# Optimization experiments

Measured on AMD Instinct MI355X. Metric: run time of the kernel, lower is better.

## Reference

```python
import jax, jax.numpy as jnp
import numpy as np

EPS = 1e-12

def _l2norm(x):
    n = jnp.sqrt(jnp.sum(x * x, axis=-1, keepdims=True))
    return x / jnp.maximum(n, EPS)

def setup_inputs() -> dict:
    key = jax.random.key(0)
    k1, k2 = jax.random.split(key)
    B, S, H = 32, 256, 768
    return {
        "query_embs": jax.random.normal(k1, (B, S, H), dtype=jnp.float32),
        "key_embs": jax.random.normal(k2, (B, S, H), dtype=jnp.float32),
        "q_mask": jnp.ones((B, S), dtype=jnp.float32),
        "k_mask": jnp.ones((B, S), dtype=jnp.float32),
        "alpha_raw": jnp.asarray(1.0, dtype=jnp.float32),
        "logit_scale": jnp.asarray(0.0, dtype=jnp.float32),  # log(1.0)
    }

def reference(query_embs, key_embs, q_mask, k_mask, alpha_raw, logit_scale):
    # query_embs, key_embs: (B, S, H); masks: (B, S)
    S = query_embs.shape[1]
    q = _l2norm(query_embs)
    k = _l2norm(key_embs)
    # all-pairs token similarity: (B, B, S, T)
    sim = jnp.einsum('ish,jth->ijst', q, k)
    # distance-decay weighting (do_distance=True, exp_decay=True)
    alpha = jax.nn.softplus(alpha_raw)
    pos = jnp.arange(S, dtype=jnp.float32)
    dist = jnp.abs(pos[:, None] - pos[None, :])  # (S, S)
    sim = sim * jnp.exp(-alpha * dist)
    # validity mask: (B, B, S, T)
    valid = (q_mask[:, None, :, None] * k_mask[None, :, None, :]) > 0
    scale = jnp.exp(logit_scale)
    neg_inf = jnp.float32(-jnp.inf)
    logits = jnp.where(valid, scale * sim, neg_inf)
    all_inf = jnp.all(logits == neg_inf, axis=-1, keepdims=True)
    safe_logits = jnp.where(all_inf, 0.0, logits)
    p = jax.nn.softmax(safe_logits, axis=-1)
    p = jnp.where(all_inf, 0.0, p)
    # softmax-weighted key aggregation: (B, B, S, H)
    agg = jnp.einsum('ijst,jth->ijsh', p, k)
    # per-token cosine score, masked mean over query tokens
    scores = jnp.einsum('ish,ijsh->ijs', q, agg) * q_mask[:, None, :]
    denom = jnp.clip(jnp.sum(q_mask, axis=-1, keepdims=True), 1.0, None)
    return jnp.sum(scores, axis=-1) / denom  # (B, B)
```

## Files before the change

### kernel.cpp

```cpp
#include <hip/hip_runtime.h>
#include <cmath>

#define BB 32
#define SS 256
#define HH 768

typedef __attribute__((ext_vector_type(8))) short bfrag8;
typedef __attribute__((ext_vector_type(4))) float accf4;

__device__ __forceinline__ unsigned short f2bf(float x) {
    unsigned int b = __float_as_uint(x);
    return (unsigned short)((b + 0x7FFFu + ((b >> 16) & 1u)) >> 16);
}

__device__ __forceinline__ float bf2f(unsigned short u) {
    return __uint_as_float(((unsigned int)u) << 16);
}

__device__ __forceinline__ void gload16(const void* g, void* l) {
    __builtin_amdgcn_global_load_lds((const __attribute__((address_space(1))) void*)g,
                                     (__attribute__((address_space(3))) void*)l, 16, 0, 0);
}


__global__ __launch_bounds__(256)
void normcvt_kernel(const float* __restrict__ Q, const float* __restrict__ K,
                    unsigned short* __restrict__ qws, unsigned short* __restrict__ kws) {
    const int wave = threadIdx.x >> 6, lane = threadIdx.x & 63;
    const bool isQ = blockIdx.x < 2048;
    const int rr = (blockIdx.x * 4 + wave) & 8191;
    const float4* src4 = isQ ? (const float4*)(Q + (size_t)rr * HH)
                             : (const float4*)(K + (size_t)rr * HH);
    float4 vv[3]; float s = 0.f;
#pragma unroll
    for (int c = 0; c < 3; ++c) {
        vv[c] = src4[lane + 64 * c];
        s += vv[c].x * vv[c].x + vv[c].y * vv[c].y + vv[c].z * vv[c].z + vv[c].w * vv[c].w;
    }
#pragma unroll
    for (int off = 1; off < 64; off <<= 1) s += __shfl_xor(s, off);
    float inv = 1.f / fmaxf(sqrtf(s), 1e-12f);

    const int b = rr >> 8, srow = rr & 255;
    unsigned short* dst = isQ ? qws : kws;
    const int e = (lane & 7) * 4;
    const int fp8 = (((e >> 3) ^ ((srow >> 1) & 3)) << 3) + (e & 7);
#pragma unroll
    for (int c = 0; c < 3; ++c) {
        int kc = (lane >> 3) + 8 * c;
        ushort4 o;
        o.x = f2bf(vv[c].x * inv); o.y = f2bf(vv[c].y * inv);
        o.z = f2bf(vv[c].z * inv); o.w = f2bf(vv[c].w * inv);
        *(ushort4*)(dst + (((size_t)b * 24 + kc) * 256 + srow) * 32 + fp8) = o;
    }
}

__global__ __launch_bounds__(256)
void ksum_kernel(const unsigned short* __restrict__ kws, const float* __restrict__ kmask,
                 unsigned short* __restrict__ ksumB) {
    __shared__ float red[4][8][4];
    const int j = blockIdx.x / 24, kc = blockIdx.x - j * 24;
    const int lane = threadIdx.x & 63, wv = threadIdx.x >> 6;
    const int tg = threadIdx.x >> 3;
    const int ec = threadIdx.x & 7;
    const unsigned short* base = kws + ((size_t)(j * 24 + kc)) * 8192;
    const float* km = kmask + j * SS;
    const int f = ec >> 1, off4 = (ec & 1) * 4;
    float s0 = 0.f, s1 = 0.f, s2 = 0.f, s3 = 0.f;
    for (int t = tg; t < 256; t += 32) {
        if (km[t] > 0.f) {
            int pos = ((f ^ ((t >> 1) & 3)) << 3) + off4;
            ushort4 v = *(const ushort4*)(base + t * 32 + pos);
            s0 += bf2f(v.x); s1 += bf2f(v.y); s2 += bf2f(v.z); s3 += bf2f(v.w);
        }
    }
#pragma unroll
    for (int off = 8; off < 64; off <<= 1) {
        s0 += __shfl_xor(s0, off); s1 += __shfl_xor(s1, off);
        s2 += __shfl_xor(s2, off); s3 += __shfl_xor(s3, off);
    }
    if ((lane >> 3) == 0) {
        red[wv][ec][0] = s0; red[wv][ec][1] = s1; red[wv][ec][2] = s2; red[wv][ec][3] = s3;
    }
    __syncthreads();
    if (threadIdx.x < 32) {
        int e2 = threadIdx.x;
        float tot = red[0][e2 >> 2][e2 & 3] + red[1][e2 >> 2][e2 & 3]
                  + red[2][e2 >> 2][e2 & 3] + red[3][e2 >> 2][e2 & 3];
        ksumB[(size_t)(j * 24 + kc) * 32 + e2] = f2bf(tot);
    }
}

__global__ __launch_bounds__(512, 2)
void mfma_kernel(const unsigned short* __restrict__ qws, const unsigned short* __restrict__ kws,
                 const float* __restrict__ qmask, const float* __restrict__ kmask,
                 const float* __restrict__ araw_p, const float* __restrict__ lscale_p,
                 const unsigned short* __restrict__ ksumB, float* __restrict__ out) {
    __shared__ __align__(16) short lq[2][8192];
    __shared__ __align__(16) short lk[2][8192];
    __shared__ __align__(16) short lKsum[2][768];
    __shared__ float sKm[2][256];
    __shared__ float wtab[13];
    __shared__ float sRed[8][2];
    __shared__ float sPart[8][2];
    __shared__ float sKcnt[2], sQden[2];

    const int tid = threadIdx.x;
    const int lane = tid & 63, w = tid >> 6;
    const int quad = lane >> 4, col = lane & 15;
    const int li = w >> 2, wq = w & 3;

    const int xcd = (int)blockIdx.x & 7, bidx = (int)blockIdx.x >> 3;
    const int ip = (xcd >> 1) * 4 + (bidx >> 3);
    const int jp = (xcd & 1) * 8 + (bidx & 7);
    const int i0 = ip * 2, j0 = jp * 2;

    const float alpha = log1pf(__expf(araw_p[0]));
    const float scale = __expf(lscale_p[0]);

    const int half = tid >> 8, hidx = tid & 255;
    float aq = qmask[(i0 + half) * SS + hidx];
    float km = kmask[(j0 + half) * SS + hidx];
    sKm[half][hidx] = km;
    float c = (km > 0.f) ? 1.f : 0.f;
#pragma unroll
    for (int off = 1; off < 64; off <<= 1) { aq += __shfl_xor(aq, off); c += __shfl_xor(c, off); }
    if (lane == 0) { sRed[w][0] = aq; sRed[w][1] = c; }
    if (tid < 13) wtab[tid] = __expf(-alpha * (float)tid);
    if (tid < 384) {
        const int jj = (tid >= 192) ? 1 : 0, e = tid - jj * 192;
        ((ushort4*)&lKsum[jj][0])[e] = ((const ushort4*)(ksumB + (size_t)(j0 + jj) * HH))[e];
    }
    __syncthreads();
    if (tid == 0) {
        sQden[0] = fmaxf(sRed[0][0] + sRed[1][0] + sRed[2][0] + sRed[3][0], 1.f);
        sQden[1] = fmaxf(sRed[4][0] + sRed[5][0] + sRed[6][0] + sRed[7][0], 1.f);
        sKcnt[0] = sRed[0][1] + sRed[1][1] + sRed[2][1] + sRed[3][1];
        sKcnt[1] = sRed[4][1] + sRed[5][1] + sRed[6][1] + sRed[7][1];
    }

    accf4 acc[2][4][3];
    accf4 accB[2][4];
#pragma unroll
    for (int lj = 0; lj < 2; ++lj) {
#pragma unroll
        for (int a = 0; a < 4; ++a) {
            accB[lj][a] = (accf4)0.f;
#pragma unroll
            for (int b = 0; b < 3; ++b) acc[lj][a][b] = (accf4)0.f;
        }
    }

    const unsigned short* psrc = (w < 4)
        ? qws + (size_t)(i0 + ((w >> 1) & 1)) * 24 * 8192
        : kws + (size_t)(j0 + ((w >> 1) & 1)) * 24 * 8192;
    unsigned short* pdst = (unsigned short*)((w < 4) ? lq[(w >> 1) & 1] : lk[(w >> 1) & 1])
                           + (w & 1) * 4096;
    const unsigned short* ssrc = psrc + (w & 1) * 4096 + lane * 8;

    const int perm8 = ((quad ^ ((col >> 1) & 3)) << 3);

    for (int kc = 0; kc < 24; ++kc) {
        __syncthreads();
        {
            const unsigned short* s = ssrc + (size_t)kc * 8192;
#pragma unroll
            for (int n = 0; n < 8; ++n)
                gload16(s + n * 512, pdst + n * 512);
        }
        __syncthreads();

        bfrag8 af[4];
#pragma unroll
        for (int sbl = 0; sbl < 4; ++sbl)
            af[sbl] = *(const bfrag8*)(&lq[li][(size_t)((wq * 4 + sbl) * 16 + col) * 32 + perm8]);
#pragma unroll
        for (int lj = 0; lj < 2; ++lj) {
            const bfrag8 kfrag = *(const bfrag8*)(&lKsum[lj][kc * 32 + quad * 8]);
            bfrag8 bfr[6];
#pragma unroll
            for (int u = 0; u < 6; ++u) {
                int tb = 4 * wq - 1 + u;
                if (tb >= 0 && tb <= 15)
                    bfr[u] = *(const bfrag8*)(&lk[lj][(size_t)(tb * 16 + col) * 32 + perm8]);
            }
#pragma unroll
            for (int sbl = 0; sbl < 4; ++sbl) {
                accB[lj][sbl] = __builtin_amdgcn_mfma_f32_16x16x32_bf16(
                    af[sbl], kfrag, accB[lj][sbl], 0, 0, 0);
#pragma unroll
                for (int dtb = 0; dtb < 3; ++dtb) {
                    int tb = 4 * wq + sbl - 1 + dtb;
                    if (tb >= 0 && tb <= 15)
                        acc[lj][sbl][dtb] = __builtin_amdgcn_mfma_f32_16x16x32_bf16(
                            af[sbl], bfr[sbl + dtb], acc[lj][sbl][dtb], 0, 0, 0);
                }
            }
        }
    }

    __syncthreads();
    float part[2] = {0.f, 0.f};
#pragma unroll
    for (int lj = 0; lj < 2; ++lj) {
        const float kcnt = sKcnt[lj];
#pragma unroll
        for (int sbl = 0; sbl < 4; ++sbl) {
            const int sbase = (wq * 4 + sbl) * 16 + quad * 4;
            float ns[4] = {0.f, 0.f, 0.f, 0.f}, ds[4] = {0.f, 0.f, 0.f, 0.f};
#pragma unroll
            for (int dtb = 0; dtb < 3; ++dtb) {
                int tb = wq * 4 + sbl - 1 + dtb;
                if (tb < 0 || tb > 15) continue;
                int t = tb * 16 + col;
                float kmv = sKm[lj][t];
#pragma unroll
                for (int reg = 0; reg < 4; ++reg) {
                    int st = sbase + reg;
                    int d = t - st;
                    bool ok = (d >= -11) && (d <= 12) && (kmv > 0.f);
                    int idx = d < 0 ? -d : d;
                    idx = ok ? idx : 0;
                    float raw = acc[lj][sbl][dtb][reg];
                    float e = ok ? expm1f(scale * raw * wtab[idx]) : 0.f;
                    ns[reg] = fmaf(e, raw, ns[reg]);
                    ds[reg] += e;
                }
            }
#pragma unroll
            for (int off = 1; off < 16; off <<= 1) {
#pragma unroll
                for (int reg = 0; reg < 4; ++reg) {
                    ns[reg] += __shfl_xor(ns[reg], off);
                    ds[reg] += __shfl_xor(ds[reg], off);
                }
            }
            if (col == 0) {
#pragma unroll
                for (int reg = 0; reg < 4; ++reg) {
                    int st = sbase + reg;
                    float qm = qmask[(i0 + li) * SS + st];
                    float bse = accB[lj][sbl][reg];
                    float dtot = ds[reg] + kcnt;
                    float v = (qm > 0.f && kcnt > 0.f) ? qm * (ns[reg] + bse) / dtot : 0.f;
                    part[lj] += v;
                }
            }
        }
    }
#pragma unroll
    for (int lj = 0; lj < 2; ++lj) {
        part[lj] += __shfl_xor(part[lj], 16);
        part[lj] += __shfl_xor(part[lj], 32);
    }
    if (lane == 0) { sPart[w][0] = part[0]; sPart[w][1] = part[1]; }
    __syncthreads();
    if (tid < 4) {
        const int tli = tid >> 1, tlj = tid & 1;
        float s = sPart[tli * 4 + 0][tlj] + sPart[tli * 4 + 1][tlj]
                + sPart[tli * 4 + 2][tlj] + sPart[tli * 4 + 3][tlj];
        out[(i0 + tli) * BB + (j0 + tlj)] = s / sQden[tli];
    }
}


extern "C" void kernel_launch(void* const* d_in, const int* in_sizes, int n_in,
                              void* d_out, int out_size, void* d_ws, size_t ws_size,
                              hipStream_t stream) {
    const float* Q      = (const float*)d_in[0];
    const float* K      = (const float*)d_in[1];
    const float* qmask  = (const float*)d_in[2];
    const float* kmask  = (const float*)d_in[3];
    const float* araw   = (const float*)d_in[4];
    const float* lscale = (const float*)d_in[5];
    float* outp = (float*)d_out;

    unsigned short* ksumB = (unsigned short*)d_ws;
    unsigned short* qws = ksumB + 24576;
    unsigned short* kws = qws + 6291456;

    normcvt_kernel<<<4096, 256, 0, stream>>>(Q, K, qws, kws);
    ksum_kernel<<<768, 256, 0, stream>>>(kws, kmask, ksumB);
    mfma_kernel<<<256, 512, 0, stream>>>(qws, kws, qmask, kmask, araw, lscale, ksumB, outp);
}
```

Baseline: 156.3 us.

## Split mfma blocks to one query batch per block, doubling grid size

Each block of the main MFMA kernel now handles one query batch against two key batches instead of a 2x2 tile, and the grid doubles from 256 to 512 blocks. Each wave covers 2 query sub-blocks instead of 4, which cuts accumulator registers, and the launch bound is raised to allow 4 blocks per CU. The aim is more occupancy and better latency hiding across the 256 CUs. In exchange, key tiles are reloaded by twice as many blocks, which raises global and L2 traffic, and the XCD-aware block mapping is dropped.

```diff
diff --git a/kernel.cpp b/kernel.cpp
--- a/kernel.cpp
+++ b/kernel.cpp
@@ -91,35 +91,33 @@
     }
 }
 
-__global__ __launch_bounds__(512, 2)
+__global__ __launch_bounds__(512, 4)
 void mfma_kernel(const unsigned short* __restrict__ qws, const unsigned short* __restrict__ kws,
                  const float* __restrict__ qmask, const float* __restrict__ kmask,
                  const float* __restrict__ araw_p, const float* __restrict__ lscale_p,
                  const unsigned short* __restrict__ ksumB, float* __restrict__ out) {
-    __shared__ __align__(16) short lq[2][8192];
+    __shared__ __align__(16) short lq[8192];
     __shared__ __align__(16) short lk[2][8192];
     __shared__ __align__(16) short lKsum[2][768];
     __shared__ float sKm[2][256];
     __shared__ float wtab[13];
     __shared__ float sRed[8][2];
     __shared__ float sPart[8][2];
-    __shared__ float sKcnt[2], sQden[2];
+    __shared__ float sKcnt[2], sQden;
 
     const int tid = threadIdx.x;
     const int lane = tid & 63, w = tid >> 6;
     const int quad = lane >> 4, col = lane & 15;
-    const int li = w >> 2, wq = w & 3;
-
-    const int xcd = (int)blockIdx.x & 7, bidx = (int)blockIdx.x >> 3;
-    const int ip = (xcd >> 1) * 4 + (bidx >> 3);
-    const int jp = (xcd & 1) * 8 + (bidx & 7);
-    const int i0 = ip * 2, j0 = jp * 2;
+
+    const int i = (int)blockIdx.x >> 4;
+    const int jp = (int)blockIdx.x & 15;
+    const int j0 = jp * 2;
 
     const float alpha = log1pf(__expf(araw_p[0]));
     const float scale = __expf(lscale_p[0]);
 
     const int half = tid >> 8, hidx = tid & 255;
-    float aq = qmask[(i0 + half) * SS + hidx];
+    float aq = qmask[i * SS + hidx];
     float km = kmask[(j0 + half) * SS + hidx];
     sKm[half][hidx] = km;
     float c = (km > 0.f) ? 1.f : 0.f;
@@ -133,64 +131,66 @@
     }
     __syncthreads();
     if (tid == 0) {
-        sQden[0] = fmaxf(sRed[0][0] + sRed[1][0] + sRed[2][0] + sRed[3][0], 1.f);
-        sQden[1] = fmaxf(sRed[4][0] + sRed[5][0] + sRed[6][0] + sRed[7][0], 1.f);
+        sQden = fmaxf(sRed[0][0] + sRed[1][0] + sRed[2][0] + sRed[3][0], 1.f);
         sKcnt[0] = sRed[0][1] + sRed[1][1] + sRed[2][1] + sRed[3][1];
         sKcnt[1] = sRed[4][1] + sRed[5][1] + sRed[6][1] + sRed[7][1];
     }
 
-    accf4 acc[2][4][3];
-    accf4 accB[2][4];
+    accf4 acc[2][2][3];
+    accf4 accB[2][2];
 #pragma unroll
     for (int lj = 0; lj < 2; ++lj) {
 #pragma unroll
-        for (int a = 0; a < 4; ++a) {
+        for (int a = 0; a < 2; ++a) {
             accB[lj][a] = (accf4)0.f;
 #pragma unroll
             for (int b = 0; b < 3; ++b) acc[lj][a][b] = (accf4)0.f;
         }
     }
 
-    const unsigned short* psrc = (w < 4)
-        ? qws + (size_t)(i0 + ((w >> 1) & 1)) * 24 * 8192
-        : kws + (size_t)(j0 + ((w >> 1) & 1)) * 24 * 8192;
-    unsigned short* pdst = (unsigned short*)((w < 4) ? lq[(w >> 1) & 1] : lk[(w >> 1) & 1])
-                           + (w & 1) * 4096;
-    const unsigned short* ssrc = psrc + (w & 1) * 4096 + lane * 8;
+    const unsigned short* qsrc  = qws + (size_t)i * 24 * 8192        + (size_t)w * 1024 + lane * 8;
+    const unsigned short* ksrc0 = kws + (size_t)j0 * 24 * 8192       + (size_t)w * 1024 + lane * 8;
+    const unsigned short* ksrc1 = kws + (size_t)(j0 + 1) * 24 * 8192 + (size_t)w * 1024 + lane * 8;
+    unsigned short* lqd  = (unsigned short*)lq    + w * 1024;
+    unsigned short* lk0d = (unsigned short*)lk[0] + w * 1024;
+    unsigned short* lk1d = (unsigned short*)lk[1] + w * 1024;
 
     const int perm8 = ((quad ^ ((col >> 1) & 3)) << 3);
 
     for (int kc = 0; kc < 24; ++kc) {
         __syncthreads();
         {
-            const unsigned short* s = ssrc + (size_t)kc * 8192;
-#pragma unroll
-            for (int n = 0; n < 8; ++n)
-                gload16(s + n * 512, pdst + n * 512);
+            const size_t o = (size_t)kc * 8192;
+            gload16(qsrc  + o,       lqd);
+            gload16(qsrc  + o + 512, lqd  + 512);
+            gload16(ksrc0 + o,       lk0d);
+            gload16(ksrc0 + o + 512, lk0d + 512);
+            gload16(ksrc1 + o,       lk1d);
+            gload16(ksrc1 + o + 512, lk1d + 512);
         }
         __syncthreads();
 
-        bfrag8 af[4];
-#pragma unroll
-        for (int sbl = 0; sbl < 4; ++sbl)
-            af[sbl] = *(const bfrag8*)(&lq[li][(size_t)((wq * 4 + sbl) * 16 + col) * 32 + perm8]);
+        bfrag8 af[2];
+#pragma unroll
+        for (int sbl = 0; sbl < 2; ++sbl)
+            af[sbl] = *(const bfrag8*)(&lq[(size_t)((2 * w + sbl) * 16 + col) * 32 + perm8]);
 #pragma unroll
         for (int lj = 0; lj < 2; ++lj) {
             const bfrag8 kfrag = *(const bfrag8*)(&lKsum[lj][kc * 32 + quad * 8]);
-            bfrag8 bfr[6];
-#pragma unroll
-            for (int u = 0; u < 6; ++u) {
-                int tb = 4 * wq - 1 + u;
+            bfrag8 bfr[4];
+#pragma unroll
+            for (int u = 0; u < 4; ++u) {
+                int tb = 2 * w - 1 + u;
                 if (tb >= 0 && tb <= 15)
                     bfr[u] = *(const bfrag8*)(&lk[lj][(size_t)(tb * 16 + col) * 32 + perm8]);
             }
 #pragma unroll
-            for (int sbl = 0; sbl < 4; ++sbl) {
+            for (int sbl = 0; sbl < 2; ++sbl) {
                 accB[lj][sbl] = __builtin_amdgcn_mfma_f32_16x16x32_bf16(
                     af[sbl], kfrag, accB[lj][sbl], 0, 0, 0);
 #pragma unroll
                 for (int dtb = 0; dtb < 3; ++dtb) {
-                    int tb = 4 * wq + sbl - 1 + dtb;
+                    int tb = 2 * w + sbl - 1 + dtb;
                     if (tb >= 0 && tb <= 15)
                         acc[lj][sbl][dtb] = __builtin_amdgcn_mfma_f32_16x16x32_bf16(
                             af[sbl], bfr[sbl + dtb], acc[lj][sbl][dtb], 0, 0, 0);
@@ -205,12 +205,12 @@
     for (int lj = 0; lj < 2; ++lj) {
         const float kcnt = sKcnt[lj];
 #pragma unroll
-        for (int sbl = 0; sbl < 4; ++sbl) {
-            const int sbase = (wq * 4 + sbl) * 16 + quad * 4;
+        for (int sbl = 0; sbl < 2; ++sbl) {
+            const int sbase = (2 * w + sbl) * 16 + quad * 4;
             float ns[4] = {0.f, 0.f, 0.f, 0.f}, ds[4] = {0.f, 0.f, 0.f, 0.f};
 #pragma unroll
             for (int dtb = 0; dtb < 3; ++dtb) {
-                int tb = wq * 4 + sbl - 1 + dtb;
+                int tb = 2 * w + sbl - 1 + dtb;
                 if (tb < 0 || tb > 15) continue;
                 int t = tb * 16 + col;
                 float kmv = sKm[lj][t];
@@ -239,7 +239,7 @@
 #pragma unroll
                 for (int reg = 0; reg < 4; ++reg) {
                     int st = sbase + reg;
-                    float qm = qmask[(i0 + li) * SS + st];
+                    float qm = qmask[i * SS + st];
                     float bse = accB[lj][sbl][reg];
                     float dtot = ds[reg] + kcnt;
                     float v = (qm > 0.f && kcnt > 0.f) ? qm * (ns[reg] + bse) / dtot : 0.f;
@@ -255,11 +255,11 @@
     }
     if (lane == 0) { sPart[w][0] = part[0]; sPart[w][1] = part[1]; }
     __syncthreads();
-    if (tid < 4) {
-        const int tli = tid >> 1, tlj = tid & 1;
-        float s = sPart[tli * 4 + 0][tlj] + sPart[tli * 4 + 1][tlj]
-                + sPart[tli * 4 + 2][tlj] + sPart[tli * 4 + 3][tlj];
-        out[(i0 + tli) * BB + (j0 + tlj)] = s / sQden[tli];
+    if (tid < 2) {
+        float s = 0.f;
+#pragma unroll
+        for (int ww = 0; ww < 8; ++ww) s += sPart[ww][tid];
+        out[i * BB + (j0 + tid)] = s / sQden;
     }
 }
 
@@ -281,5 +281,5 @@
 
     normcvt_kernel<<<4096, 256, 0, stream>>>(Q, K, qws, kws);
     ksum_kernel<<<768, 256, 0, stream>>>(kws, kmask, ksumB);
-    mfma_kernel<<<256, 512, 0, stream>>>(qws, kws, qmask, kmask, araw, lscale, ksumB, outp);
-}
+    mfma_kernel<<<512, 512, 0, stream>>>(qws, kws, qmask, kmask, araw, lscale, ksumB, outp);
+}
```

After: 145.6 us, median of 2. 6.8% less time.
